# Performance work log

Hardware: AMD Instinct MI355X
Metric: run time of the kernel (lower is better)

Reference implementation:

```python
import jax, jax.numpy as jnp
import numpy as np

ALPHA = 0.5
PATH_LEN = 7  # 1 start entity + 3 (module, entity) hops
NUM_ENTITIES = 200000
EMBED = 128
NUM_MOD = 64
HIDDEN = 512
OUT_DIM = 64
BATCH = 8192


def setup_inputs() -> dict:
    key = jax.random.key(0)
    ks = jax.random.split(key, 8)
    stdv = 1.0 / np.sqrt(EMBED)
    return {
        "entity_embeds": jax.random.normal(ks[0], (NUM_ENTITIES, EMBED), jnp.float32) * 0.05,
        "W_mods": jax.random.uniform(ks[1], (NUM_MOD, EMBED, EMBED), jnp.float32, -stdv, stdv),
        "W1": jax.random.normal(ks[2], (HIDDEN, EMBED), jnp.float32) * stdv,
        "b1": jax.random.normal(ks[3], (HIDDEN,), jnp.float32) * 0.01,
        "W2": jax.random.normal(ks[4], (OUT_DIM, HIDDEN), jnp.float32) * (1.0 / np.sqrt(HIDDEN)),
        "b2": jax.random.normal(ks[5], (OUT_DIM,), jnp.float32) * 0.01,
        "entity_ids": jax.random.randint(ks[6], (BATCH, 4), 0, NUM_ENTITIES, jnp.int64 if jax.config.jax_enable_x64 else jnp.int32),
        "module_ids": jax.random.randint(ks[7], (BATCH, 3), 0, NUM_MOD, jnp.int64 if jax.config.jax_enable_x64 else jnp.int32),
    }


def reference(entity_embeds, W_mods, W1, b1, W2, b2, entity_ids, module_ids):
    # Batched version of ModuleNet.forward over a batch of fixed-length-7 paths.
    x = entity_embeds[entity_ids[:, 0]]  # [B, E] start entity embedding
    bias = x
    for h in range(3):  # hops over (module_id, entity_id) pairs
        Wm = W_mods[module_ids[:, h]]          # [B, E, E] per-row weight gather
        bias = entity_embeds[entity_ids[:, h + 1]]  # [B, E]
        x = jax.nn.relu(jnp.einsum('boi,bi->bo', Wm, x) + bias)
    w = 1.0 / (PATH_LEN * ALPHA)
    out = (1.0 - w) * bias + w * x  # [B, E]
    # classifier: Linear -> ReLU -> Linear
    h1 = jax.nn.relu(out @ W1.T + b1)
    logits = h1 @ W2.T + b2  # [B, OUT_DIM]
    return logits
```

## Files before the change

kernel.cpp:

```cpp
#include <hip/hip_runtime.h>

namespace {

typedef short bf16x8 __attribute__((ext_vector_type(8)));
typedef float f32x4 __attribute__((ext_vector_type(4)));

constexpr int BATCH = 8192;
constexpr int NMOD  = 64;
constexpr int CAP   = 256;
constexpr int CSTR  = 16;
constexpr float WB  = 1.0f / (7.0f * 0.5f);

constexpr size_t OFF_WHI = 0;
constexpr size_t OFF_WLO = 524288;
constexpr size_t OFF_XH0 = 1048576;
constexpr size_t OFF_XL0 = 1572864;
constexpr size_t OFF_XH1 = 2097152;
constexpr size_t OFF_XL1 = 2621440;
constexpr size_t OFF_W1H = 3145728;
constexpr size_t OFF_W1L = 3178496;
constexpr size_t OFF_W2H = 3211264;
constexpr size_t OFF_W2L = 3227648;
constexpr size_t OFF_CNT = 3244032;
constexpr size_t OFF_BKT = 3247104;

__device__ __forceinline__ ushort f2bf(float x) {
  unsigned u = __builtin_bit_cast(unsigned, x);
  u += 0x7FFFu + ((u >> 16) & 1u);
  return (ushort)(u >> 16);
}
__device__ __forceinline__ float bf2f(ushort h) {
  return __builtin_bit_cast(float, ((unsigned)h) << 16);
}
__device__ __forceinline__ void cvt8(const float* v, bf16x8& hi, bf16x8& lo) {
#pragma unroll
  for (int j = 0; j < 8; ++j) {
    const float x = v[j];
    const ushort h = f2bf(x);
    hi[j] = (short)h;
    lo[j] = (short)f2bf(x - bf2f(h));
  }
}

__global__ __launch_bounds__(256) void k_prep(const float* __restrict__ Wm,
                                              const float* __restrict__ W1,
                                              const float* __restrict__ W2,
                                              const int* __restrict__ mids,
                                              float* __restrict__ ws) {
  const int bx = blockIdx.x;
  const int tid = threadIdx.x;
  if (bx < 560) {
    const float* src;
    ushort *dh, *dl;
    size_t i8;
    if (bx < 512) {
      src = Wm; dh = (ushort*)(ws + OFF_WHI); dl = (ushort*)(ws + OFF_WLO);
      i8 = (size_t)bx * 256 + tid;
    } else if (bx < 544) {
      src = W1; dh = (ushort*)(ws + OFF_W1H); dl = (ushort*)(ws + OFF_W1L);
      i8 = (size_t)(bx - 512) * 256 + tid;
    } else {
      src = W2; dh = (ushort*)(ws + OFF_W2H); dl = (ushort*)(ws + OFF_W2L);
      i8 = (size_t)(bx - 544) * 256 + tid;
    }
    float v[8];
    *(float4*)&v[0] = *(const float4*)&src[i8 * 8];
    *(float4*)&v[4] = *(const float4*)&src[i8 * 8 + 4];
    bf16x8 hi, lo;
    cvt8(v, hi, lo);
    *(bf16x8*)&dh[i8 * 8] = hi;
    *(bf16x8*)&dl[i8 * 8] = lo;
  } else {
    const int idx = (bx - 560) * 256 + tid;
    if (idx < BATCH * 3) {
      const int b = idx / 3, h = idx - b * 3;
      const int m = mids[idx];
      int* cnt = (int*)(ws + OFF_CNT);
      int* bkt = (int*)(ws + OFF_BKT);
      const int pos = atomicAdd(&cnt[(h * NMOD + m) * CSTR], 1);
      bkt[(h * NMOD + m) * CAP + pos] = b;
    }
  }
}

template <int HOP>
__global__ __launch_bounds__(512, 1) void k_hop(const float* __restrict__ E,
                                                const int* __restrict__ eids,
                                                float* __restrict__ ws) {
  const int m = blockIdx.x >> 2, sl = blockIdx.x & 3;
  const int cn = ((const int*)(ws + OFF_CNT))[(HOP * NMOD + m) * CSTR];
  const int r0 = sl * 64;
  if (r0 >= cn) return;
  const int nr = min(64, cn - r0);

  __shared__ ushort wh[128 * 72];
  __shared__ ushort wl[128 * 72];
  __shared__ int rows[64], esrc[64], ebia[64];

  const int tid = threadIdx.x;
  const ushort* WhiG = (const ushort*)(ws + OFF_WHI) + (size_t)m * 16384;
  const ushort* WloG = (const ushort*)(ws + OFF_WLO) + (size_t)m * 16384;
  const int* bkt = (const int*)(ws + OFF_BKT) + (HOP * NMOD + m) * CAP + r0;
  const ushort* XHp = (const ushort*)(ws + (HOP == 2 ? OFF_XH1 : OFF_XH0));
  const ushort* XLp = (const ushort*)(ws + (HOP == 2 ? OFF_XL1 : OFF_XL0));
  ushort* XHn = (ushort*)(ws + (HOP == 1 ? OFF_XH1 : OFF_XH0));
  ushort* XLn = (ushort*)(ws + (HOP == 1 ? OFF_XL1 : OFF_XL0));

  if (tid < 64) {
    const int b = bkt[tid < nr ? tid : 0];
    rows[tid] = b;
    esrc[tid] = (HOP == 0) ? eids[b * 4] : b;
    ebia[tid] = eids[b * 4 + HOP + 1];
  }

  const int w = tid >> 6, l = tid & 63;
  const int lg = l >> 4, lr = l & 15;
  const int g = w & 3;
  const int f0 = (w >> 2) * 4;

  f32x4 acc[4] = {};

#pragma unroll
  for (int p = 0; p < 2; ++p) {
    __syncthreads();
    for (int e = tid; e < 128 * 8; e += 512) {
      const int c = e >> 3, s = e & 7;
      *(bf16x8*)&wh[c * 72 + s * 8] =
          *(const bf16x8*)&WhiG[(size_t)c * 128 + p * 64 + s * 8];
      *(bf16x8*)&wl[c * 72 + s * 8] =
          *(const bf16x8*)&WloG[(size_t)c * 128 + p * 64 + s * 8];
    }
    __syncthreads();

    bf16x8 ah[2], al[2];
    {
      const int row = g * 16 + lr;
#pragma unroll
      for (int s = 0; s < 2; ++s) {
        const int k0 = p * 64 + s * 32 + lg * 8;
        if (HOP == 0) {
          const float* sp = E + (size_t)esrc[row] * 128;
          float v[8];
          *(float4*)&v[0] = *(const float4*)&sp[k0];
          *(float4*)&v[4] = *(const float4*)&sp[k0 + 4];
          cvt8(v, ah[s], al[s]);
        } else {
          const size_t xo = (size_t)esrc[row] * 128 + k0;
          ah[s] = *(const bf16x8*)&XHp[xo];
          al[s] = *(const bf16x8*)&XLp[xo];
        }
      }
    }

#pragma unroll
    for (int f = 0; f < 4; ++f) {
      const int c = (f0 + f) * 16 + lr;
#pragma unroll
      for (int s = 0; s < 2; ++s) {
        const bf16x8 bh = *(const bf16x8*)&wh[c * 72 + s * 32 + lg * 8];
        const bf16x8 bl = *(const bf16x8*)&wl[c * 72 + s * 32 + lg * 8];
        acc[f] = __builtin_amdgcn_mfma_f32_16x16x32_bf16(ah[s], bh, acc[f], 0, 0, 0);
        acc[f] = __builtin_amdgcn_mfma_f32_16x16x32_bf16(al[s], bh, acc[f], 0, 0, 0);
        acc[f] = __builtin_amdgcn_mfma_f32_16x16x32_bf16(ah[s], bl, acc[f], 0, 0, 0);
      }
    }
  }

#pragma unroll
  for (int q = 0; q < 4; ++q) {
    const int row = g * 16 + lg * 4 + q;
    if (row < nr) {
      const int b = rows[row];
      const float* bp = E + (size_t)ebia[row] * 128;
      const size_t ob = (size_t)b * 128;
#pragma unroll
      for (int f = 0; f < 4; ++f) {
        const int col = (f0 + f) * 16 + lr;
        const float bias = bp[col];
        float v = fmaxf(acc[f][q] + bias, 0.f);
        if (HOP == 2) v = (1.f - WB) * bias + WB * v;
        const ushort h = f2bf(v);
        XHn[ob + col] = h;
        XLn[ob + col] = f2bf(v - bf2f(h));
      }
    }
  }
}

constexpr int HSTR = 520;
constexpr int WSTR = 136;
__global__ __launch_bounds__(256, 2) void k_mlp(const float* __restrict__ b1,
                                                const float* __restrict__ b2,
                                                float* __restrict__ ws,
                                                float* __restrict__ out) {
  __shared__ ushort w1h[64 * WSTR];
  __shared__ ushort w1l[64 * WSTR];
  __shared__ ushort hh[16 * HSTR];
  __shared__ ushort hl[16 * HSTR];
  const int tid = threadIdx.x;
  const int row0 = blockIdx.x * 16;
  const ushort* XH = (const ushort*)(ws + OFF_XH0);
  const ushort* XL = (const ushort*)(ws + OFF_XL0);
  const ushort* W1H = (const ushort*)(ws + OFF_W1H);
  const ushort* W1L = (const ushort*)(ws + OFF_W1L);
  const ushort* W2H = (const ushort*)(ws + OFF_W2H);
  const ushort* W2L = (const ushort*)(ws + OFF_W2L);

  const int w = tid >> 6, l = tid & 63;
  const int lg = l >> 4, lr = l & 15;

  bf16x8 ah[4], al[4];
#pragma unroll
  for (int s = 0; s < 4; ++s) {
    const size_t xo = (size_t)(row0 + lr) * 128 + s * 32 + lg * 8;
    ah[s] = *(const bf16x8*)&XH[xo];
    al[s] = *(const bf16x8*)&XL[xo];
  }

  for (int ch = 0; ch < 8; ++ch) {
    __syncthreads();
    for (int e = tid; e < 64 * 16; e += 256) {
      const int c = e >> 4, s8 = e & 15;
      const size_t go = (size_t)(ch * 64 + c) * 128 + s8 * 8;
      *(bf16x8*)&w1h[c * WSTR + s8 * 8] = *(const bf16x8*)&W1H[go];
      *(bf16x8*)&w1l[c * WSTR + s8 * 8] = *(const bf16x8*)&W1L[go];
    }
    __syncthreads();

    const int cl = w * 16 + lr;
    f32x4 a = {};
#pragma unroll
    for (int s = 0; s < 4; ++s) {
      const bf16x8 bh = *(const bf16x8*)&w1h[cl * WSTR + s * 32 + lg * 8];
      const bf16x8 bl = *(const bf16x8*)&w1l[cl * WSTR + s * 32 + lg * 8];
      a = __builtin_amdgcn_mfma_f32_16x16x32_bf16(ah[s], bh, a, 0, 0, 0);
      a = __builtin_amdgcn_mfma_f32_16x16x32_bf16(al[s], bh, a, 0, 0, 0);
      a = __builtin_amdgcn_mfma_f32_16x16x32_bf16(ah[s], bl, a, 0, 0, 0);
    }
    const int c = ch * 64 + w * 16 + lr;
    const float bb = b1[c];
#pragma unroll
    for (int q = 0; q < 4; ++q) {
      const int r = lg * 4 + q;
      const float v = fmaxf(a[q] + bb, 0.f);
      const ushort h = f2bf(v);
      hh[r * HSTR + c] = h;
      hl[r * HSTR + c] = f2bf(v - bf2f(h));
    }
  }
  __syncthreads();

  f32x4 acc2 = {};
#pragma unroll 4
  for (int s = 0; s < 16; ++s) {
    const size_t wo = (size_t)(w * 16 + lr) * 512 + s * 32 + lg * 8;
    const bf16x8 a2h = *(const bf16x8*)&W2H[wo];
    const bf16x8 a2l = *(const bf16x8*)&W2L[wo];
    const int ko = s * 32 + lg * 8;
    const bf16x8 b2h = *(const bf16x8*)&hh[lr * HSTR + ko];
    const bf16x8 b2l = *(const bf16x8*)&hl[lr * HSTR + ko];
    acc2 = __builtin_amdgcn_mfma_f32_16x16x32_bf16(a2h, b2h, acc2, 0, 0, 0);
    acc2 = __builtin_amdgcn_mfma_f32_16x16x32_bf16(a2l, b2h, acc2, 0, 0, 0);
    acc2 = __builtin_amdgcn_mfma_f32_16x16x32_bf16(a2h, b2l, acc2, 0, 0, 0);
  }
  const float4 bb2 = *(const float4*)&b2[w * 16 + lg * 4];
  float4 o;
  o.x = acc2[0] + bb2.x;
  o.y = acc2[1] + bb2.y;
  o.z = acc2[2] + bb2.z;
  o.w = acc2[3] + bb2.w;
  *(float4*)&out[(size_t)(row0 + lr) * 64 + w * 16 + lg * 4] = o;
}

}

extern "C" void kernel_launch(void* const* d_in, const int* in_sizes, int n_in,
                              void* d_out, int out_size, void* d_ws,
                              size_t ws_size, hipStream_t stream) {
  const float* E  = (const float*)d_in[0];
  const float* Wm = (const float*)d_in[1];
  const float* W1 = (const float*)d_in[2];
  const float* b1 = (const float*)d_in[3];
  const float* W2 = (const float*)d_in[4];
  const float* b2 = (const float*)d_in[5];
  const int* eids = (const int*)d_in[6];
  const int* mids = (const int*)d_in[7];
  float* out = (float*)d_out;
  float* ws = (float*)d_ws;

  (void)hipMemsetAsync((char*)d_ws + OFF_CNT * sizeof(float), 0,
                       192 * CSTR * sizeof(int), stream);
  k_prep<<<dim3(656), dim3(256), 0, stream>>>(Wm, W1, W2, mids, ws);
  k_hop<0><<<dim3(256), dim3(512), 0, stream>>>(E, eids, ws);
  k_hop<1><<<dim3(256), dim3(512), 0, stream>>>(E, eids, ws);
  k_hop<2><<<dim3(256), dim3(512), 0, stream>>>(E, eids, ws);
  k_mlp<<<dim3(512), dim3(256), 0, stream>>>(b1, b2, ws, out);
}
```

Baseline: 71.91 us.

## Replace atomic bucketing with ballot-based per-module scan and restructure MLP tiling

Bucketing of rows by (hop, module) is now done by one block per pair, which scans all module ids with wave ballots and prefix popcounts instead of global atomics. This removes the counter memset launch and makes the bucket order deterministic, at the cost of each of 192 blocks reading the whole module-id array. The MLP kernel now handles 32 rows per 512-thread block and reads W1 fragments straight from global memory (cache) into MFMA operands, dropping the shared-memory staging and per-chunk barriers. The trade-off is more registers for the eight accumulators and redundant global W1 reads across blocks.

```diff
diff --git a/kernel.cpp b/kernel.cpp
--- a/kernel.cpp
+++ b/kernel.cpp
@@ -47,6 +47,7 @@
                                               const float* __restrict__ W2,
                                               const int* __restrict__ mids,
                                               float* __restrict__ ws) {
+  __shared__ int wsum[4];
   const int bx = blockIdx.x;
   const int tid = threadIdx.x;
   if (bx < 560) {
@@ -71,15 +72,28 @@
     *(bf16x8*)&dh[i8 * 8] = hi;
     *(bf16x8*)&dl[i8 * 8] = lo;
   } else {
-    const int idx = (bx - 560) * 256 + tid;
-    if (idx < BATCH * 3) {
-      const int b = idx / 3, h = idx - b * 3;
-      const int m = mids[idx];
-      int* cnt = (int*)(ws + OFF_CNT);
-      int* bkt = (int*)(ws + OFF_BKT);
-      const int pos = atomicAdd(&cnt[(h * NMOD + m) * CSTR], 1);
-      bkt[(h * NMOD + m) * CAP + pos] = b;
-    }
+    const int hm = bx - 560;
+    const int h = hm / NMOD, m = hm & 63;
+    int* cnt = (int*)(ws + OFF_CNT);
+    int* bkt = (int*)(ws + OFF_BKT) + hm * CAP;
+    const int wv = tid >> 6, ln = tid & 63;
+    int count = 0;
+    for (int it = 0; it < BATCH / 256; ++it) {
+      const int b = it * 256 + tid;
+      const bool hit = (mids[b * 3 + h] == m);
+      const unsigned long long mask = __ballot(hit);
+      const int pre = __popcll(mask & ((1ull << ln) - 1ull));
+      if (ln == 0) wsum[wv] = __popcll(mask);
+      __syncthreads();
+      int wbase = count;
+#pragma unroll
+      for (int u = 0; u < 4; ++u)
+        if (u < wv) wbase += wsum[u];
+      if (hit) bkt[wbase + pre] = b;
+      count += wsum[0] + wsum[1] + wsum[2] + wsum[3];
+      __syncthreads();
+    }
+    if (tid == 0) cnt[hm * CSTR] = count;
   }
 }
 
@@ -188,17 +202,14 @@
 }
 
 constexpr int HSTR = 520;
-constexpr int WSTR = 136;
-__global__ __launch_bounds__(256, 2) void k_mlp(const float* __restrict__ b1,
+__global__ __launch_bounds__(512, 2) void k_mlp(const float* __restrict__ b1,
                                                 const float* __restrict__ b2,
                                                 float* __restrict__ ws,
                                                 float* __restrict__ out) {
-  __shared__ ushort w1h[64 * WSTR];
-  __shared__ ushort w1l[64 * WSTR];
-  __shared__ ushort hh[16 * HSTR];
-  __shared__ ushort hl[16 * HSTR];
+  __shared__ ushort hh[32 * HSTR];
+  __shared__ ushort hl[32 * HSTR];
   const int tid = threadIdx.x;
-  const int row0 = blockIdx.x * 16;
+  const int row0 = blockIdx.x * 32;
   const ushort* XH = (const ushort*)(ws + OFF_XH0);
   const ushort* XL = (const ushort*)(ws + OFF_XL0);
   const ushort* W1H = (const ushort*)(ws + OFF_W1H);
@@ -209,40 +220,36 @@
   const int w = tid >> 6, l = tid & 63;
   const int lg = l >> 4, lr = l & 15;
 
+  const int rowg = w & 1, colq = w >> 1;
   bf16x8 ah[4], al[4];
 #pragma unroll
   for (int s = 0; s < 4; ++s) {
-    const size_t xo = (size_t)(row0 + lr) * 128 + s * 32 + lg * 8;
+    const size_t xo = (size_t)(row0 + rowg * 16 + lr) * 128 + s * 32 + lg * 8;
     ah[s] = *(const bf16x8*)&XH[xo];
     al[s] = *(const bf16x8*)&XL[xo];
   }
-
-  for (int ch = 0; ch < 8; ++ch) {
-    __syncthreads();
-    for (int e = tid; e < 64 * 16; e += 256) {
-      const int c = e >> 4, s8 = e & 15;
-      const size_t go = (size_t)(ch * 64 + c) * 128 + s8 * 8;
-      *(bf16x8*)&w1h[c * WSTR + s8 * 8] = *(const bf16x8*)&W1H[go];
-      *(bf16x8*)&w1l[c * WSTR + s8 * 8] = *(const bf16x8*)&W1L[go];
-    }
-    __syncthreads();
-
-    const int cl = w * 16 + lr;
-    f32x4 a = {};
+  f32x4 acc[8] = {};
+#pragma unroll
+  for (int f = 0; f < 8; ++f) {
+    const int c = colq * 128 + f * 16 + lr;
 #pragma unroll
     for (int s = 0; s < 4; ++s) {
-      const bf16x8 bh = *(const bf16x8*)&w1h[cl * WSTR + s * 32 + lg * 8];
-      const bf16x8 bl = *(const bf16x8*)&w1l[cl * WSTR + s * 32 + lg * 8];
-      a = __builtin_amdgcn_mfma_f32_16x16x32_bf16(ah[s], bh, a, 0, 0, 0);
-      a = __builtin_amdgcn_mfma_f32_16x16x32_bf16(al[s], bh, a, 0, 0, 0);
-      a = __builtin_amdgcn_mfma_f32_16x16x32_bf16(ah[s], bl, a, 0, 0, 0);
-    }
-    const int c = ch * 64 + w * 16 + lr;
+      const size_t wo = (size_t)c * 128 + s * 32 + lg * 8;
+      const bf16x8 bh = *(const bf16x8*)&W1H[wo];
+      const bf16x8 bl = *(const bf16x8*)&W1L[wo];
+      acc[f] = __builtin_amdgcn_mfma_f32_16x16x32_bf16(ah[s], bh, acc[f], 0, 0, 0);
+      acc[f] = __builtin_amdgcn_mfma_f32_16x16x32_bf16(al[s], bh, acc[f], 0, 0, 0);
+      acc[f] = __builtin_amdgcn_mfma_f32_16x16x32_bf16(ah[s], bl, acc[f], 0, 0, 0);
+    }
+  }
+#pragma unroll
+  for (int f = 0; f < 8; ++f) {
+    const int c = colq * 128 + f * 16 + lr;
     const float bb = b1[c];
 #pragma unroll
     for (int q = 0; q < 4; ++q) {
-      const int r = lg * 4 + q;
-      const float v = fmaxf(a[q] + bb, 0.f);
+      const int r = rowg * 16 + lg * 4 + q;
+      const float v = fmaxf(acc[f][q] + bb, 0.f);
       const ushort h = f2bf(v);
       hh[r * HSTR + c] = h;
       hl[r * HSTR + c] = f2bf(v - bf2f(h));
@@ -250,26 +257,27 @@
   }
   __syncthreads();
 
+  const int ob16 = (w & 3) * 16, rb = w >> 2;
   f32x4 acc2 = {};
 #pragma unroll 4
   for (int s = 0; s < 16; ++s) {
-    const size_t wo = (size_t)(w * 16 + lr) * 512 + s * 32 + lg * 8;
+    const size_t wo = (size_t)(ob16 + lr) * 512 + s * 32 + lg * 8;
     const bf16x8 a2h = *(const bf16x8*)&W2H[wo];
     const bf16x8 a2l = *(const bf16x8*)&W2L[wo];
     const int ko = s * 32 + lg * 8;
-    const bf16x8 b2h = *(const bf16x8*)&hh[lr * HSTR + ko];
-    const bf16x8 b2l = *(const bf16x8*)&hl[lr * HSTR + ko];
+    const bf16x8 b2h = *(const bf16x8*)&hh[(rb * 16 + lr) * HSTR + ko];
+    const bf16x8 b2l = *(const bf16x8*)&hl[(rb * 16 + lr) * HSTR + ko];
     acc2 = __builtin_amdgcn_mfma_f32_16x16x32_bf16(a2h, b2h, acc2, 0, 0, 0);
     acc2 = __builtin_amdgcn_mfma_f32_16x16x32_bf16(a2l, b2h, acc2, 0, 0, 0);
     acc2 = __builtin_amdgcn_mfma_f32_16x16x32_bf16(a2h, b2l, acc2, 0, 0, 0);
   }
-  const float4 bb2 = *(const float4*)&b2[w * 16 + lg * 4];
+  const float4 bb2 = *(const float4*)&b2[ob16 + lg * 4];
   float4 o;
   o.x = acc2[0] + bb2.x;
   o.y = acc2[1] + bb2.y;
   o.z = acc2[2] + bb2.z;
   o.w = acc2[3] + bb2.w;
-  *(float4*)&out[(size_t)(row0 + lr) * 64 + w * 16 + lg * 4] = o;
+  *(float4*)&out[(size_t)(row0 + rb * 16 + lr) * 64 + ob16 + lg * 4] = o;
 }
 
 }
@@ -288,11 +296,9 @@
   float* out = (float*)d_out;
   float* ws = (float*)d_ws;
 
-  (void)hipMemsetAsync((char*)d_ws + OFF_CNT * sizeof(float), 0,
-                       192 * CSTR * sizeof(int), stream);
-  k_prep<<<dim3(656), dim3(256), 0, stream>>>(Wm, W1, W2, mids, ws);
+  k_prep<<<dim3(752), dim3(256), 0, stream>>>(Wm, W1, W2, mids, ws);
   k_hop<0><<<dim3(256), dim3(512), 0, stream>>>(E, eids, ws);
   k_hop<1><<<dim3(256), dim3(512), 0, stream>>>(E, eids, ws);
   k_hop<2><<<dim3(256), dim3(512), 0, stream>>>(E, eids, ws);
-  k_mlp<<<dim3(512), dim3(256), 0, stream>>>(b1, b2, ws, out);
-}
+  k_mlp<<<dim3(256), dim3(512), 0, stream>>>(b1, b2, ws, out);
+}
```

Measured after the change: 77.05 us. 1.07x slower.
